# Kernel tuning notes

Measured on AMD Instinct MI355X. Metric: run time of the kernel, lower is better.

Reference implementation:

```python
import jax, jax.numpy as jnp
import numpy as np

N_NODES = 50000


def gcn_conv(x, W, b, src, dst, num_nodes):
    """PyG GCNConv: x' = D^{-1/2} (A + I) D^{-1/2} (x W) + b.

    Transform first (smaller feature dim work is the same either way here),
    then propagate with symmetric normalization including self-loops.
    """
    h = x @ W  # [N, F_out]
    # degree with self-loops: deg[i] = 1 + #incoming edges
    ones = jnp.ones(dst.shape[0], dtype=h.dtype)
    deg = jax.ops.segment_sum(ones, dst, num_segments=num_nodes) + 1.0  # [N]
    dinv_sqrt = jax.lax.rsqrt(deg)
    norm = dinv_sqrt[src] * dinv_sqrt[dst]  # [E]
    msg = h[src] * norm[:, None]  # [E, F_out]
    agg = jax.ops.segment_sum(msg, dst, num_segments=num_nodes)
    # self-loop contribution: norm_ii = deg_i^{-1/2} * deg_i^{-1/2} = 1/deg_i
    agg = agg + h * (dinv_sqrt * dinv_sqrt)[:, None]
    return agg + b


def setup_inputs() -> dict:
    key = jax.random.key(0)
    ks = jax.random.split(key, 11)
    N, E = N_NODES, 1600000
    in_ch, oc = 128, 32
    dims = [in_ch, 8 * oc, 4 * oc, 2 * oc, oc]  # 128 -> 256 -> 128 -> 64 -> 32
    x = jax.random.normal(ks[0], (N, in_ch), dtype=jnp.float32)
    edge_index = jax.random.randint(ks[1], (2, E), 0, N, dtype=jnp.int64)
    params = {}
    for i, (din, dout) in enumerate(zip(dims[:-1], dims[1:])):
        scale = 1.0 / np.sqrt(din)
        params[f"W{i+1}"] = jax.random.uniform(ks[2 + 2 * i], (din, dout), jnp.float32, -scale, scale)
        params[f"b{i+1}"] = jnp.zeros((dout,), dtype=jnp.float32)
    return {"x": x, "edge_index": edge_index, **params}


def reference(x, edge_index, W1, b1, W2, b2, W3, b3, W4, b4):
    src, dst = edge_index[0], edge_index[1]
    h = jax.nn.relu(gcn_conv(x, W1, b1, src, dst, N_NODES))
    h = jax.nn.relu(gcn_conv(h, W2, b2, src, dst, N_NODES))
    h = jax.nn.relu(gcn_conv(h, W3, b3, src, dst, N_NODES))
    h = jax.nn.relu(gcn_conv(h, W4, b4, src, dst, N_NODES))
    # Dropout(p=0.5) is identity at eval time.
    return h
```

## Files before the change

### kernel.cpp

```cpp
#include <hip/hip_runtime.h>
#include <stdint.h>


#define NN      50000
#define CAP     96
#define BSZ     256
#define NB      196
#define NSLICEA 256
#define CAPSEG  96
#define NBIN    16
#define LPAD    98

#define PREP_DINV_B   196
#define PREP_B2FS_B   6250
#define PREP_WT_T     2368
#define PREP_WT_B     10

typedef int   iv4   __attribute__((ext_vector_type(4)));
typedef short bfv8  __attribute__((ext_vector_type(8)));
typedef float fv4   __attribute__((ext_vector_type(4)));

__device__ __forceinline__ float bflo(uint32_t u) {
    uint32_t b = u << 16; float f; __builtin_memcpy(&f, &b, 4); return f;
}
__device__ __forceinline__ float bfhi(uint32_t u) {
    uint32_t b = u & 0xffff0000u; float f; __builtin_memcpy(&f, &b, 4); return f;
}
__device__ __forceinline__ unsigned short f2bf(float f) {
    uint32_t u; __builtin_memcpy(&u, &f, 4);
    return (unsigned short)((u + 0x7fffu + ((u >> 16) & 1u)) >> 16);
}
__device__ __forceinline__ uint32_t packbf(float lo, float hi) {
    return (uint32_t)f2bf(lo) | ((uint32_t)f2bf(hi) << 16);
}

__global__ __launch_bounds__(256) void k_bucket(uint32_t* __restrict__ seg,
                                                int* __restrict__ cnts,
                                                const int* __restrict__ src,
                                                const int* __restrict__ dst,
                                                int E) {
    __shared__ int cnt[NB];
    const int slice = blockIdx.x;
    for (int i = threadIdx.x; i < NB; i += 256) cnt[i] = 0;
    __syncthreads();
    int per = (E + NSLICEA - 1) / NSLICEA;
    per = (per + 3) & ~3;
    const int e0 = slice * per;
    uint32_t* const segp = seg + (long)slice * NB * CAPSEG;
    if (e0 < E) {
        const int e1 = (e0 + per < E) ? e0 + per : E;
        const int nv = (e1 - e0) & ~3;
        for (int t = e0 + (int)threadIdx.x * 4; t + 4 <= e0 + nv; t += 256 * 4) {
            iv4 dd = __builtin_nontemporal_load((const iv4*)(dst + t));
            iv4 ss = __builtin_nontemporal_load((const iv4*)(src + t));
#pragma unroll
            for (int q = 0; q < 4; ++q) {
                int d = dd[q];
                int b = d >> 8;
                uint32_t val = ((uint32_t)ss[q] << 8) | (uint32_t)(d & 255);
                int slot = atomicAdd(&cnt[b], 1);
                if (slot < CAPSEG) segp[b * CAPSEG + slot] = val;
            }
        }
        int tt = e0 + nv + (int)threadIdx.x;
        if (tt < e1) {
            int d = __builtin_nontemporal_load(dst + tt);
            int s = __builtin_nontemporal_load(src + tt);
            int b = d >> 8;
            uint32_t val = ((uint32_t)s << 8) | (uint32_t)(d & 255);
            int slot = atomicAdd(&cnt[b], 1);
            if (slot < CAPSEG) segp[b * CAPSEG + slot] = val;
        }
    }
    __syncthreads();
    for (int i = threadIdx.x; i < NB; i += 256)
        cnts[slice * NB + i] = (cnt[i] < CAPSEG) ? cnt[i] : CAPSEG;
}

__global__ __launch_bounds__(256) void k_build(unsigned short* __restrict__ pcsr,
                                               int* __restrict__ cur,
                                               const uint32_t* __restrict__ seg,
                                               const int* __restrict__ cnts,
                                               int N) {
    __shared__ unsigned short lrow[BSZ][LPAD];
    __shared__ int bcnt[BSZ][NBIN + 1];
    __shared__ int ldeg[BSZ];
    const int b = blockIdx.x;
    for (int i = threadIdx.x; i < BSZ * (NBIN + 1); i += 256)
        ((int*)bcnt)[i] = 0;
    __syncthreads();

    const int slice = threadIdx.x;
    const int n = cnts[slice * NB + b];
    const uint32_t* sp = seg + ((long)slice * NB + b) * CAPSEG;

    for (int i = 0; i < n; ++i) {
        uint32_t val = sp[i];
        int d = (int)(val & 255u);
        int s = (int)(val >> 8);
        atomicAdd(&bcnt[d][s >> 12], 1);
    }
    __syncthreads();

    {
        const int r = threadIdx.x;
        int acc = 0;
#pragma unroll
        for (int k = 0; k < NBIN; ++k) {
            int c = bcnt[r][k];
            bcnt[r][k] = acc;
            acc += c;
        }
        ldeg[r] = acc;
    }
    __syncthreads();

    for (int i = 0; i < n; ++i) {
        uint32_t val = sp[i];
        int d = (int)(val & 255u);
        int s = (int)(val >> 8);
        int slot = atomicAdd(&bcnt[d][s >> 12], 1);
        if (slot < CAP) lrow[d][slot] = (unsigned short)s;
    }
    __syncthreads();

    const int node0 = b * BSZ;
    int nrows = N - node0;
    if (nrows > BSZ) nrows = BSZ;
    const int total = nrows * (CAP / 2);
    for (int idx = threadIdx.x; idx < total; idx += 256) {
        int r = idx / (CAP / 2);
        int c = idx - r * (CAP / 2);
        ((uint32_t*)(pcsr + (long)(node0 + r) * CAP))[c] =
            ((const uint32_t*)lrow[r])[c];
    }
    for (int r = threadIdx.x; r < nrows; r += 256) cur[node0 + r] = ldeg[r];
}

__device__ __forceinline__ void wt_pack(unsigned short* __restrict__ wt,
                                        const float* __restrict__ W,
                                        int dout, int t) {
    int kc = t / dout, n = t - kc * dout;
    unsigned short* o = wt + (long)t * 32;
#pragma unroll
    for (int kk = 0; kk < 32; ++kk) o[kk] = f2bf(W[(kc * 32 + kk) * dout + n]);
}

__global__ __launch_bounds__(256) void k_prep(float* __restrict__ dinv,
                                              const int* __restrict__ cur,
                                              unsigned short* __restrict__ U,
                                              const float* __restrict__ x,
                                              unsigned short* __restrict__ Wt1,
                                              const float* __restrict__ W1,
                                              unsigned short* __restrict__ Wt2,
                                              const float* __restrict__ W2,
                                              unsigned short* __restrict__ Wt3,
                                              const float* __restrict__ W3,
                                              unsigned short* __restrict__ Wt4,
                                              const float* __restrict__ W4) {
    const int b = blockIdx.x;
    if (b < PREP_DINV_B) {
        int t = b * 256 + threadIdx.x;
        if (t < NN) dinv[t] = 1.0f / sqrtf((float)cur[t] + 1.0f);
    } else if (b < PREP_DINV_B + PREP_B2FS_B) {
        int t = (b - PREP_DINV_B) * 256 + threadIdx.x;
        float w = 1.0f / sqrtf((float)cur[t >> 5] + 1.0f);
        float4 v = reinterpret_cast<const float4*>(x)[t];
        ushort4 o;
        o.x = f2bf(v.x * w); o.y = f2bf(v.y * w);
        o.z = f2bf(v.z * w); o.w = f2bf(v.w * w);
        reinterpret_cast<ushort4*>(U)[t] = o;
    } else {
        int t = (b - PREP_DINV_B - PREP_B2FS_B) * 256 + threadIdx.x;
        if (t < 1024)      wt_pack(Wt1, W1, 256, t);
        else if (t < 2048) wt_pack(Wt2, W2, 128, t - 1024);
        else if (t < 2304) wt_pack(Wt3, W3, 64, t - 2048);
        else if (t < PREP_WT_T) wt_pack(Wt4, W4, 32, t - 2304);
    }
}

template <int D, int BR, int OUTBF>
__global__ __launch_bounds__(256) void k_pullq(void* __restrict__ outv,
                                               const unsigned short* __restrict__ Hb,
                                               const unsigned short* __restrict__ pcsr,
                                               const int* __restrict__ deg,
                                               const float* __restrict__ dinv,
                                               const float* __restrict__ bias,
                                               int n) {
    constexpr int TPN = D / 8;
    constexpr int NPB = 256 / TPN;
    const int node = blockIdx.x * NPB + threadIdx.x / TPN;
    const int f8 = threadIdx.x % TPN;
    if (node >= n) return;
    const float wd = dinv[node];
    const uint4* __restrict__ Hv = (const uint4*)Hb;
    uint4 ps = Hv[(long)node * TPN + f8];
    float a0 = bflo(ps.x), a1 = bfhi(ps.x);
    float a2 = bflo(ps.y), a3 = bfhi(ps.y);
    float a4 = bflo(ps.z), a5 = bfhi(ps.z);
    float a6 = bflo(ps.w), a7 = bfhi(ps.w);
    int dg = deg[node];
    if (dg > CAP) dg = CAP;
    const unsigned short* __restrict__ row = pcsr + (long)node * CAP;
    int j = 0;
    for (; j + 4 <= dg; j += 4) {
        ushort4 ii = *(const ushort4*)(row + j);
        uint4 p0 = Hv[(long)ii.x * TPN + f8];
        uint4 p1 = Hv[(long)ii.y * TPN + f8];
        uint4 p2 = Hv[(long)ii.z * TPN + f8];
        uint4 p3 = Hv[(long)ii.w * TPN + f8];
        a0 += bflo(p0.x) + bflo(p1.x) + bflo(p2.x) + bflo(p3.x);
        a1 += bfhi(p0.x) + bfhi(p1.x) + bfhi(p2.x) + bfhi(p3.x);
        a2 += bflo(p0.y) + bflo(p1.y) + bflo(p2.y) + bflo(p3.y);
        a3 += bfhi(p0.y) + bfhi(p1.y) + bfhi(p2.y) + bfhi(p3.y);
        a4 += bflo(p0.z) + bflo(p1.z) + bflo(p2.z) + bflo(p3.z);
        a5 += bfhi(p0.z) + bfhi(p1.z) + bfhi(p2.z) + bfhi(p3.z);
        a6 += bflo(p0.w) + bflo(p1.w) + bflo(p2.w) + bflo(p3.w);
        a7 += bfhi(p0.w) + bfhi(p1.w) + bfhi(p2.w) + bfhi(p3.w);
    }
    for (; j < dg; ++j) {
        uint4 p = Hv[(long)row[j] * TPN + f8];
        a0 += bflo(p.x); a1 += bfhi(p.x);
        a2 += bflo(p.y); a3 += bfhi(p.y);
        a4 += bflo(p.z); a5 += bfhi(p.z);
        a6 += bflo(p.w); a7 += bfhi(p.w);
    }
    a0 *= wd; a1 *= wd; a2 *= wd; a3 *= wd;
    a4 *= wd; a5 *= wd; a6 *= wd; a7 *= wd;
    if (BR) {
        float4 b0 = ((const float4*)bias)[2 * f8];
        float4 b1 = ((const float4*)bias)[2 * f8 + 1];
        a0 = fmaxf(a0 + b0.x, 0.f); a1 = fmaxf(a1 + b0.y, 0.f);
        a2 = fmaxf(a2 + b0.z, 0.f); a3 = fmaxf(a3 + b0.w, 0.f);
        a4 = fmaxf(a4 + b1.x, 0.f); a5 = fmaxf(a5 + b1.y, 0.f);
        a6 = fmaxf(a6 + b1.z, 0.f); a7 = fmaxf(a7 + b1.w, 0.f);
    }
    if (OUTBF) {
        uint4 o;
        o.x = packbf(a0, a1); o.y = packbf(a2, a3);
        o.z = packbf(a4, a5); o.w = packbf(a6, a7);
        ((uint4*)outv)[(long)node * TPN + f8] = o;
    } else {
        float4 o0; o0.x = a0; o0.y = a1; o0.z = a2; o0.w = a3;
        float4 o1; o1.x = a4; o1.y = a5; o1.z = a6; o1.w = a7;
        ((float4*)outv)[(long)node * (D / 4) + 2 * f8] = o0;
        ((float4*)outv)[(long)node * (D / 4) + 2 * f8 + 1] = o1;
    }
}

template <int DIN, int NT, int BIAS_RELU, int OUTBF, int SCALE>
__global__ __launch_bounds__(256) void k_mm(const unsigned short* __restrict__ Xb,
                                            const unsigned short* __restrict__ Wt,
                                            const float* __restrict__ bias,
                                            const float* __restrict__ dinv,
                                            void* __restrict__ outv,
                                            int N, int dout) {
    constexpr int KI = DIN / 32;
    const int lane = threadIdx.x & 63;
    const int wv   = threadIdx.x >> 6;
    const int m0   = blockIdx.x * 64 + wv * 16;
    const int n0   = blockIdx.y * (NT * 16);
    const int l15  = lane & 15;
    const int quad = lane >> 4;

    int mrow = m0 + l15;
    if (mrow >= N) mrow = N - 1;
    const unsigned short* xp = Xb + (long)mrow * DIN + quad * 8;
    const unsigned short* wp = Wt + (long)(n0 + l15) * 32 + quad * 8;

    fv4 acc[NT];
#pragma unroll
    for (int t = 0; t < NT; ++t) acc[t] = (fv4){0.f, 0.f, 0.f, 0.f};

#pragma unroll
    for (int kc = 0; kc < KI; ++kc) {
        bfv8 a = *(const bfv8*)(xp + kc * 32);
#pragma unroll
        for (int t = 0; t < NT; ++t) {
            bfv8 b = *(const bfv8*)(wp + (long)kc * dout * 32 + t * 16 * 32);
            acc[t] = __builtin_amdgcn_mfma_f32_16x16x32_bf16(a, b, acc[t], 0, 0, 0);
        }
    }

    float sc[4];
#pragma unroll
    for (int r = 0; r < 4; ++r) {
        int m = m0 + quad * 4 + r;
        sc[r] = SCALE ? dinv[(m < N) ? m : (N - 1)] : 1.0f;
    }

#pragma unroll
    for (int t = 0; t < NT; ++t) {
        const int col = n0 + t * 16 + l15;
        float bb = BIAS_RELU ? bias[col] : 0.f;
#pragma unroll
        for (int r = 0; r < 4; ++r) {
            int m = m0 + quad * 4 + r;
            if (m < N) {
                float v = acc[t][r];
                if (BIAS_RELU) v = fmaxf(v + bb, 0.f);
                if (SCALE) v *= sc[r];
                if (OUTBF)
                    ((unsigned short*)outv)[(long)m * dout + col] = f2bf(v);
                else
                    ((float*)outv)[(long)m * dout + col] = v;
            }
        }
    }
}

extern "C" void kernel_launch(void* const* d_in, const int* in_sizes, int n_in,
                              void* d_out, int out_size, void* d_ws, size_t ws_size,
                              hipStream_t stream) {
    const int N = NN;
    const int E = in_sizes[1] / 2;

    const float* x  = (const float*)d_in[0];
    const int* ei   = (const int*)d_in[1];
    const int* src  = ei;
    const int* dst  = ei + E;
    const float* W1 = (const float*)d_in[2];
    const float* b1 = (const float*)d_in[3];
    const float* W2 = (const float*)d_in[4];
    const float* b2 = (const float*)d_in[5];
    const float* W3 = (const float*)d_in[6];
    const float* b3 = (const float*)d_in[7];
    const float* W4 = (const float*)d_in[8];
    const float* b4 = (const float*)d_in[9];

    float* dinv = (float*)d_ws;
    int*   cur  = (int*)(dinv + N);
    unsigned short* U    = (unsigned short*)(cur + N);
    unsigned short* V    = U + (long)N * 256;
    unsigned short* pcsr = V + (long)N * 256;
    unsigned short* Wt1  = pcsr + (long)N * CAP;
    unsigned short* Wt2  = Wt1 + 128 * 256;
    unsigned short* Wt3  = Wt2 + 256 * 128;
    unsigned short* Wt4  = Wt3 + 128 * 64;

    uint32_t* seg  = (uint32_t*)U;
    int*      cnts = (int*)(seg + (long)NSLICEA * NB * CAPSEG);

    (void)n_in; (void)out_size; (void)ws_size;

    const int GX = (N + 63) / 64;

    k_bucket<<<NSLICEA, 256, 0, stream>>>(seg, cnts, src, dst, E);
    k_build<<<NB, 256, 0, stream>>>(pcsr, cur, seg, cnts, N);
    k_prep<<<PREP_DINV_B + PREP_B2FS_B + PREP_WT_B, 256, 0, stream>>>(
        dinv, cur, U, x, Wt1, W1, Wt2, W2, Wt3, W3, Wt4, W4);

    k_pullq<128, 0, 1><<<(N + 15) / 16, 256, 0, stream>>>(V, U, pcsr, cur, dinv, nullptr, N);
    k_mm<128, 4, 1, 1, 0><<<dim3(GX, 4), 256, 0, stream>>>(V, Wt1, b1, dinv, U, N, 256);

    k_mm<256, 4, 0, 1, 1><<<dim3(GX, 2), 256, 0, stream>>>(U, Wt2, nullptr, dinv, V, N, 128);
    k_pullq<128, 1, 1><<<(N + 15) / 16, 256, 0, stream>>>(U, V, pcsr, cur, dinv, b2, N);

    k_mm<128, 4, 0, 1, 1><<<dim3(GX, 1), 256, 0, stream>>>(U, Wt3, nullptr, dinv, V, N, 64);
    k_pullq<64, 1, 1><<<(N + 31) / 32, 256, 0, stream>>>(U, V, pcsr, cur, dinv, b3, N);

    k_mm<64, 2, 0, 1, 1><<<dim3(GX, 1), 256, 0, stream>>>(U, Wt4, nullptr, dinv, V, N, 32);
    k_pullq<32, 1, 0><<<(N + 63) / 64, 256, 0, stream>>>(d_out, V, pcsr, cur, dinv, b4, N);
}
```

Measured before the change: 308.6 us.

## Fuse layer-1 aggregation with its matmul and interleave two nodes per thread

Adds a kernel that gathers neighbour features for 32 nodes, stages the normalised bf16 rows in shared memory, and runs the 128->256 MFMA matmul with bias and ReLU in the same block. This removes the layer-1 intermediate write and read to global memory and one kernel launch. The 128-wide aggregation for layer 2 now gives each thread two nodes and interleaves their gathers to keep more loads in flight. The cost is fewer nodes per block in the fused kernel and heavier register and LDS use, which may lower occupancy, and the final output is written with scattered 2-byte stores.

```diff
diff --git a/kernel.cpp b/kernel.cpp
--- a/kernel.cpp
+++ b/kernel.cpp
@@ -10,6 +10,7 @@
 #define CAPSEG  96
 #define NBIN    16
 #define LPAD    98
+#define LSTR    68
 
 #define PREP_DINV_B   196
 #define PREP_B2FS_B   6250
@@ -96,12 +97,9 @@
 
     for (int i = 0; i < n; ++i) {
         uint32_t val = sp[i];
-        int d = (int)(val & 255u);
-        int s = (int)(val >> 8);
-        atomicAdd(&bcnt[d][s >> 12], 1);
-    }
-    __syncthreads();
-
+        atomicAdd(&bcnt[val & 255u][(val >> 8) >> 12], 1);
+    }
+    __syncthreads();
     {
         const int r = threadIdx.x;
         int acc = 0;
@@ -114,7 +112,6 @@
         ldeg[r] = acc;
     }
     __syncthreads();
-
     for (int i = 0; i < n; ++i) {
         uint32_t val = sp[i];
         int d = (int)(val & 255u);
@@ -179,6 +176,185 @@
     }
 }
 
+template <int TPN>
+__device__ __forceinline__ void gather4(const uint4* __restrict__ Hv,
+                                        const unsigned short* __restrict__ row,
+                                        int j, int f8, float* a) {
+    ushort4 ii = *(const ushort4*)(row + j);
+    uint4 p0 = Hv[(long)ii.x * TPN + f8];
+    uint4 p1 = Hv[(long)ii.y * TPN + f8];
+    uint4 p2 = Hv[(long)ii.z * TPN + f8];
+    uint4 p3 = Hv[(long)ii.w * TPN + f8];
+    a[0] += bflo(p0.x) + bflo(p1.x) + bflo(p2.x) + bflo(p3.x);
+    a[1] += bfhi(p0.x) + bfhi(p1.x) + bfhi(p2.x) + bfhi(p3.x);
+    a[2] += bflo(p0.y) + bflo(p1.y) + bflo(p2.y) + bflo(p3.y);
+    a[3] += bfhi(p0.y) + bfhi(p1.y) + bfhi(p2.y) + bfhi(p3.y);
+    a[4] += bflo(p0.z) + bflo(p1.z) + bflo(p2.z) + bflo(p3.z);
+    a[5] += bfhi(p0.z) + bfhi(p1.z) + bfhi(p2.z) + bfhi(p3.z);
+    a[6] += bflo(p0.w) + bflo(p1.w) + bflo(p2.w) + bflo(p3.w);
+    a[7] += bfhi(p0.w) + bfhi(p1.w) + bfhi(p2.w) + bfhi(p3.w);
+}
+template <int TPN>
+__device__ __forceinline__ void gather1(const uint4* __restrict__ Hv,
+                                        const unsigned short* __restrict__ row,
+                                        int j, int f8, float* a) {
+    uint4 p = Hv[(long)row[j] * TPN + f8];
+    a[0] += bflo(p.x); a[1] += bfhi(p.x);
+    a[2] += bflo(p.y); a[3] += bfhi(p.y);
+    a[4] += bflo(p.z); a[5] += bfhi(p.z);
+    a[6] += bflo(p.w); a[7] += bfhi(p.w);
+}
+
+__device__ __forceinline__ void pull2_core(const uint4* __restrict__ Hv,
+                                           const unsigned short* __restrict__ pcsr,
+                                           const int* __restrict__ deg,
+                                           int nA, int nB, int n, int f8,
+                                           float* aA, float* aB) {
+    int dgA = 0, dgB = 0;
+    const unsigned short *rowA = pcsr, *rowB = pcsr;
+    if (nA < n) {
+        uint4 ps = Hv[(long)nA * 16 + f8];
+        aA[0] = bflo(ps.x); aA[1] = bfhi(ps.x); aA[2] = bflo(ps.y); aA[3] = bfhi(ps.y);
+        aA[4] = bflo(ps.z); aA[5] = bfhi(ps.z); aA[6] = bflo(ps.w); aA[7] = bfhi(ps.w);
+        dgA = deg[nA]; if (dgA > CAP) dgA = CAP;
+        rowA = pcsr + (long)nA * CAP;
+    }
+    if (nB < n) {
+        uint4 ps = Hv[(long)nB * 16 + f8];
+        aB[0] = bflo(ps.x); aB[1] = bfhi(ps.x); aB[2] = bflo(ps.y); aB[3] = bfhi(ps.y);
+        aB[4] = bflo(ps.z); aB[5] = bfhi(ps.z); aB[6] = bflo(ps.w); aB[7] = bfhi(ps.w);
+        dgB = deg[nB]; if (dgB > CAP) dgB = CAP;
+        rowB = pcsr + (long)nB * CAP;
+    }
+    int ja = 0, jb = 0;
+    while (ja + 4 <= dgA && jb + 4 <= dgB) {
+        gather4<16>(Hv, rowA, ja, f8, aA); ja += 4;
+        gather4<16>(Hv, rowB, jb, f8, aB); jb += 4;
+    }
+    for (; ja + 4 <= dgA; ja += 4) gather4<16>(Hv, rowA, ja, f8, aA);
+    for (; jb + 4 <= dgB; jb += 4) gather4<16>(Hv, rowB, jb, f8, aB);
+    for (; ja < dgA; ++ja) gather1<16>(Hv, rowA, ja, f8, aA);
+    for (; jb < dgB; ++jb) gather1<16>(Hv, rowB, jb, f8, aB);
+}
+
+template <int BR, int OUTBF>
+__global__ __launch_bounds__(256) void k_pullq2(void* __restrict__ outv,
+                                                const unsigned short* __restrict__ Hb,
+                                                const unsigned short* __restrict__ pcsr,
+                                                const int* __restrict__ deg,
+                                                const float* __restrict__ dinv,
+                                                const float* __restrict__ bias,
+                                                int n) {
+    const int slot = threadIdx.x >> 4;
+    const int f8   = threadIdx.x & 15;
+    const int base = blockIdx.x * 32;
+    const int nA = base + slot, nB = base + slot + 16;
+    const uint4* __restrict__ Hv = (const uint4*)Hb;
+    float aA[8] = {0,0,0,0,0,0,0,0}, aB[8] = {0,0,0,0,0,0,0,0};
+    pull2_core(Hv, pcsr, deg, nA, nB, n, f8, aA, aB);
+
+    float b8[8];
+    if (BR) {
+        float4 b0 = ((const float4*)bias)[2 * f8];
+        float4 b1 = ((const float4*)bias)[2 * f8 + 1];
+        b8[0] = b0.x; b8[1] = b0.y; b8[2] = b0.z; b8[3] = b0.w;
+        b8[4] = b1.x; b8[5] = b1.y; b8[6] = b1.z; b8[7] = b1.w;
+    }
+#pragma unroll
+    for (int pass = 0; pass < 2; ++pass) {
+        int node = pass ? nB : nA;
+        float* a = pass ? aB : aA;
+        if (node >= n) continue;
+        float wd = dinv[node];
+#pragma unroll
+        for (int k = 0; k < 8; ++k) {
+            a[k] *= wd;
+            if (BR) a[k] = fmaxf(a[k] + b8[k], 0.f);
+        }
+        if (OUTBF) {
+            uint4 o;
+            o.x = packbf(a[0], a[1]); o.y = packbf(a[2], a[3]);
+            o.z = packbf(a[4], a[5]); o.w = packbf(a[6], a[7]);
+            ((uint4*)outv)[(long)node * 16 + f8] = o;
+        } else {
+            float4 o0 = {a[0], a[1], a[2], a[3]};
+            float4 o1 = {a[4], a[5], a[6], a[7]};
+            ((float4*)outv)[(long)node * 32 + 2 * f8] = o0;
+            ((float4*)outv)[(long)node * 32 + 2 * f8 + 1] = o1;
+        }
+    }
+}
+
+__global__ __launch_bounds__(256) void k_pullmm1(unsigned short* __restrict__ outH,
+                                                 const unsigned short* __restrict__ Hb,
+                                                 const unsigned short* __restrict__ pcsr,
+                                                 const int* __restrict__ deg,
+                                                 const float* __restrict__ dinv,
+                                                 const unsigned short* __restrict__ Wt,
+                                                 const float* __restrict__ bias,
+                                                 int n) {
+    __shared__ uint32_t lds[32 * LSTR];
+    const int slot = threadIdx.x >> 4;
+    const int f8   = threadIdx.x & 15;
+    const int base = blockIdx.x * 32;
+    const int nA = base + slot, nB = base + slot + 16;
+    const uint4* __restrict__ Hv = (const uint4*)Hb;
+    float aA[8] = {0,0,0,0,0,0,0,0}, aB[8] = {0,0,0,0,0,0,0,0};
+    pull2_core(Hv, pcsr, deg, nA, nB, n, f8, aA, aB);
+
+    {
+        float wdA = (nA < n) ? dinv[nA] : 0.f;
+        float wdB = (nB < n) ? dinv[nB] : 0.f;
+        uint32_t* pa = &lds[slot * LSTR + f8 * 4];
+        uint32_t* pb = &lds[(slot + 16) * LSTR + f8 * 4];
+        pa[0] = packbf(aA[0] * wdA, aA[1] * wdA);
+        pa[1] = packbf(aA[2] * wdA, aA[3] * wdA);
+        pa[2] = packbf(aA[4] * wdA, aA[5] * wdA);
+        pa[3] = packbf(aA[6] * wdA, aA[7] * wdA);
+        pb[0] = packbf(aB[0] * wdB, aB[1] * wdB);
+        pb[1] = packbf(aB[2] * wdB, aB[3] * wdB);
+        pb[2] = packbf(aB[4] * wdB, aB[5] * wdB);
+        pb[3] = packbf(aB[6] * wdB, aB[7] * wdB);
+    }
+    __syncthreads();
+
+    const int lane = threadIdx.x & 63;
+    const int wv   = threadIdx.x >> 6;
+    const int l15  = lane & 15;
+    const int quad = lane >> 4;
+    const int n0   = wv * 64;
+    fv4 acc[2][4];
+#pragma unroll
+    for (int mt = 0; mt < 2; ++mt)
+#pragma unroll
+        for (int t = 0; t < 4; ++t) acc[mt][t] = (fv4){0.f, 0.f, 0.f, 0.f};
+
+#pragma unroll
+    for (int kc = 0; kc < 4; ++kc) {
+        bfv8 a0 = *(const bfv8*)((const unsigned short*)&lds[l15 * LSTR] + quad * 8 + kc * 32);
+        bfv8 a1 = *(const bfv8*)((const unsigned short*)&lds[(16 + l15) * LSTR] + quad * 8 + kc * 32);
+#pragma unroll
+        for (int t = 0; t < 4; ++t) {
+            bfv8 b = *(const bfv8*)(Wt + (long)(n0 + t * 16 + l15) * 32 + quad * 8 + (long)kc * 256 * 32);
+            acc[0][t] = __builtin_amdgcn_mfma_f32_16x16x32_bf16(a0, b, acc[0][t], 0, 0, 0);
+            acc[1][t] = __builtin_amdgcn_mfma_f32_16x16x32_bf16(a1, b, acc[1][t], 0, 0, 0);
+        }
+    }
+#pragma unroll
+    for (int mt = 0; mt < 2; ++mt)
+#pragma unroll
+        for (int t = 0; t < 4; ++t) {
+            int col = n0 + t * 16 + l15;
+            float bb = bias[col];
+#pragma unroll
+            for (int r = 0; r < 4; ++r) {
+                int m = base + mt * 16 + quad * 4 + r;
+                if (m < n)
+                    outH[(long)m * 256 + col] = f2bf(fmaxf(acc[mt][t][r] + bb, 0.f));
+            }
+        }
+}
+
 template <int D, int BR, int OUTBF>
 __global__ __launch_bounds__(256) void k_pullq(void* __restrict__ outv,
                                                const unsigned short* __restrict__ Hb,
@@ -195,54 +371,33 @@
     const float wd = dinv[node];
     const uint4* __restrict__ Hv = (const uint4*)Hb;
     uint4 ps = Hv[(long)node * TPN + f8];
-    float a0 = bflo(ps.x), a1 = bfhi(ps.x);
-    float a2 = bflo(ps.y), a3 = bfhi(ps.y);
-    float a4 = bflo(ps.z), a5 = bfhi(ps.z);
-    float a6 = bflo(ps.w), a7 = bfhi(ps.w);
+    float a[8];
+    a[0] = bflo(ps.x); a[1] = bfhi(ps.x); a[2] = bflo(ps.y); a[3] = bfhi(ps.y);
+    a[4] = bflo(ps.z); a[5] = bfhi(ps.z); a[6] = bflo(ps.w); a[7] = bfhi(ps.w);
     int dg = deg[node];
     if (dg > CAP) dg = CAP;
     const unsigned short* __restrict__ row = pcsr + (long)node * CAP;
     int j = 0;
-    for (; j + 4 <= dg; j += 4) {
-        ushort4 ii = *(const ushort4*)(row + j);
-        uint4 p0 = Hv[(long)ii.x * TPN + f8];
-        uint4 p1 = Hv[(long)ii.y * TPN + f8];
-        uint4 p2 = Hv[(long)ii.z * TPN + f8];
-        uint4 p3 = Hv[(long)ii.w * TPN + f8];
-        a0 += bflo(p0.x) + bflo(p1.x) + bflo(p2.x) + bflo(p3.x);
-        a1 += bfhi(p0.x) + bfhi(p1.x) + bfhi(p2.x) + bfhi(p3.x);
-        a2 += bflo(p0.y) + bflo(p1.y) + bflo(p2.y) + bflo(p3.y);
-        a3 += bfhi(p0.y) + bfhi(p1.y) + bfhi(p2.y) + bfhi(p3.y);
-        a4 += bflo(p0.z) + bflo(p1.z) + bflo(p2.z) + bflo(p3.z);
-        a5 += bfhi(p0.z) + bfhi(p1.z) + bfhi(p2.z) + bfhi(p3.z);
-        a6 += bflo(p0.w) + bflo(p1.w) + bflo(p2.w) + bflo(p3.w);
-        a7 += bfhi(p0.w) + bfhi(p1.w) + bfhi(p2.w) + bfhi(p3.w);
-    }
-    for (; j < dg; ++j) {
-        uint4 p = Hv[(long)row[j] * TPN + f8];
-        a0 += bflo(p.x); a1 += bfhi(p.x);
-        a2 += bflo(p.y); a3 += bfhi(p.y);
-        a4 += bflo(p.z); a5 += bfhi(p.z);
-        a6 += bflo(p.w); a7 += bfhi(p.w);
-    }
-    a0 *= wd; a1 *= wd; a2 *= wd; a3 *= wd;
-    a4 *= wd; a5 *= wd; a6 *= wd; a7 *= wd;
+    for (; j + 4 <= dg; j += 4) gather4<TPN>(Hv, row, j, f8, a);
+    for (; j < dg; ++j) gather1<TPN>(Hv, row, j, f8, a);
+#pragma unroll
+    for (int k = 0; k < 8; ++k) a[k] *= wd;
     if (BR) {
         float4 b0 = ((const float4*)bias)[2 * f8];
         float4 b1 = ((const float4*)bias)[2 * f8 + 1];
-        a0 = fmaxf(a0 + b0.x, 0.f); a1 = fmaxf(a1 + b0.y, 0.f);
-        a2 = fmaxf(a2 + b0.z, 0.f); a3 = fmaxf(a3 + b0.w, 0.f);
-        a4 = fmaxf(a4 + b1.x, 0.f); a5 = fmaxf(a5 + b1.y, 0.f);
-        a6 = fmaxf(a6 + b1.z, 0.f); a7 = fmaxf(a7 + b1.w, 0.f);
+        a[0] = fmaxf(a[0] + b0.x, 0.f); a[1] = fmaxf(a[1] + b0.y, 0.f);
+        a[2] = fmaxf(a[2] + b0.z, 0.f); a[3] = fmaxf(a[3] + b0.w, 0.f);
+        a[4] = fmaxf(a[4] + b1.x, 0.f); a[5] = fmaxf(a[5] + b1.y, 0.f);
+        a[6] = fmaxf(a[6] + b1.z, 0.f); a[7] = fmaxf(a[7] + b1.w, 0.f);
     }
     if (OUTBF) {
         uint4 o;
-        o.x = packbf(a0, a1); o.y = packbf(a2, a3);
-        o.z = packbf(a4, a5); o.w = packbf(a6, a7);
+        o.x = packbf(a[0], a[1]); o.y = packbf(a[2], a[3]);
+        o.z = packbf(a[4], a[5]); o.w = packbf(a[6], a[7]);
         ((uint4*)outv)[(long)node * TPN + f8] = o;
     } else {
-        float4 o0; o0.x = a0; o0.y = a1; o0.z = a2; o0.w = a3;
-        float4 o1; o1.x = a4; o1.y = a5; o1.z = a6; o1.w = a7;
+        float4 o0 = {a[0], a[1], a[2], a[3]};
+        float4 o1 = {a[4], a[5], a[6], a[7]};
         ((float4*)outv)[(long)node * (D / 4) + 2 * f8] = o0;
         ((float4*)outv)[(long)node * (D / 4) + 2 * f8 + 1] = o1;
     }
@@ -344,21 +499,21 @@
     (void)n_in; (void)out_size; (void)ws_size;
 
     const int GX = (N + 63) / 64;
+    const int GP2 = (N + 31) / 32;
 
     k_bucket<<<NSLICEA, 256, 0, stream>>>(seg, cnts, src, dst, E);
     k_build<<<NB, 256, 0, stream>>>(pcsr, cur, seg, cnts, N);
     k_prep<<<PREP_DINV_B + PREP_B2FS_B + PREP_WT_B, 256, 0, stream>>>(
         dinv, cur, U, x, Wt1, W1, Wt2, W2, Wt3, W3, Wt4, W4);
 
-    k_pullq<128, 0, 1><<<(N + 15) / 16, 256, 0, stream>>>(V, U, pcsr, cur, dinv, nullptr, N);
-    k_mm<128, 4, 1, 1, 0><<<dim3(GX, 4), 256, 0, stream>>>(V, Wt1, b1, dinv, U, N, 256);
-
-    k_mm<256, 4, 0, 1, 1><<<dim3(GX, 2), 256, 0, stream>>>(U, Wt2, nullptr, dinv, V, N, 128);
-    k_pullq<128, 1, 1><<<(N + 15) / 16, 256, 0, stream>>>(U, V, pcsr, cur, dinv, b2, N);
-
-    k_mm<128, 4, 0, 1, 1><<<dim3(GX, 1), 256, 0, stream>>>(U, Wt3, nullptr, dinv, V, N, 64);
-    k_pullq<64, 1, 1><<<(N + 31) / 32, 256, 0, stream>>>(U, V, pcsr, cur, dinv, b3, N);
-
-    k_mm<64, 2, 0, 1, 1><<<dim3(GX, 1), 256, 0, stream>>>(U, Wt4, nullptr, dinv, V, N, 32);
-    k_pullq<32, 1, 0><<<(N + 63) / 64, 256, 0, stream>>>(d_out, V, pcsr, cur, dinv, b4, N);
-}
+    k_pullmm1<<<GP2, 256, 0, stream>>>(V, U, pcsr, cur, dinv, Wt1, b1, N);
+
+    k_mm<256, 4, 0, 1, 1><<<dim3(GX, 2), 256, 0, stream>>>(V, Wt2, nullptr, dinv, U, N, 128);
+    k_pullq2<1, 1><<<GP2, 256, 0, stream>>>(V, U, pcsr, cur, dinv, b2, N);
+
+    k_mm<128, 4, 0, 1, 1><<<dim3(GX, 1), 256, 0, stream>>>(V, Wt3, nullptr, dinv, U, N, 64);
+    k_pullq<64, 1, 1><<<(N + 31) / 32, 256, 0, stream>>>(V, U, pcsr, cur, dinv, b3, N);
+
+    k_mm<64, 2, 0, 1, 1><<<dim3(GX, 1), 256, 0, stream>>>(V, Wt4, nullptr, dinv, U, N, 32);
+    k_pullq<32, 1, 0><<<(N + 63) / 64, 256, 0, stream>>>(d_out, U, pcsr, cur, dinv, b4, N);
+}
```

Result: slower. 324.9 us (+5.3%).

## Fuse prep, propagation and matmul stages into one cooperative persistent kernel

Applied to the files above, without the earlier changes.

Replaces the nine separate prep/pull/matmul launches with a single cooperative kernel that loops over virtual blocks and uses grid-wide syncs between stages. The aim is to remove per-launch overhead and the tail idle time at each kernel boundary. The grid size comes from an occupancy query with a minimum-occupancy hint of five blocks per CU, and the old multi-launch path is kept as a fallback if the cooperative launch fails. In exchange, grid.sync costs are added, __restrict__ qualifiers are dropped, and the fused kernel may suffer higher register pressure.

```diff
diff --git a/kernel.cpp b/kernel.cpp
--- a/kernel.cpp
+++ b/kernel.cpp
@@ -1,5 +1,8 @@
 #include <hip/hip_runtime.h>
+#include <hip/hip_cooperative_groups.h>
 #include <stdint.h>
+
+namespace cg = cooperative_groups;
 
 
 #define NN      50000
@@ -15,6 +18,12 @@
 #define PREP_B2FS_B   6250
 #define PREP_WT_T     2368
 #define PREP_WT_B     10
+#define PREP_TOT_B    (PREP_DINV_B + PREP_B2FS_B + PREP_WT_B)
+
+#define GXMM    782
+#define VB_P128 3125
+#define VB_P64  1563
+#define VB_P32  782
 
 typedef int   iv4   __attribute__((ext_vector_type(4)));
 typedef short bfv8  __attribute__((ext_vector_type(8)));
@@ -96,12 +105,9 @@
 
     for (int i = 0; i < n; ++i) {
         uint32_t val = sp[i];
-        int d = (int)(val & 255u);
-        int s = (int)(val >> 8);
-        atomicAdd(&bcnt[d][s >> 12], 1);
-    }
-    __syncthreads();
-
+        atomicAdd(&bcnt[val & 255u][(val >> 8) >> 12], 1);
+    }
+    __syncthreads();
     {
         const int r = threadIdx.x;
         int acc = 0;
@@ -114,7 +120,6 @@
         ldeg[r] = acc;
     }
     __syncthreads();
-
     for (int i = 0; i < n; ++i) {
         uint32_t val = sp[i];
         int d = (int)(val & 255u);
@@ -137,8 +142,7 @@
     for (int r = threadIdx.x; r < nrows; r += 256) cur[node0 + r] = ldeg[r];
 }
 
-__device__ __forceinline__ void wt_pack(unsigned short* __restrict__ wt,
-                                        const float* __restrict__ W,
+__device__ __forceinline__ void wt_pack(unsigned short* wt, const float* W,
                                         int dout, int t) {
     int kc = t / dout, n = t - kc * dout;
     unsigned short* o = wt + (long)t * 32;
@@ -146,24 +150,18 @@
     for (int kk = 0; kk < 32; ++kk) o[kk] = f2bf(W[(kc * 32 + kk) * dout + n]);
 }
 
-__global__ __launch_bounds__(256) void k_prep(float* __restrict__ dinv,
-                                              const int* __restrict__ cur,
-                                              unsigned short* __restrict__ U,
-                                              const float* __restrict__ x,
-                                              unsigned short* __restrict__ Wt1,
-                                              const float* __restrict__ W1,
-                                              unsigned short* __restrict__ Wt2,
-                                              const float* __restrict__ W2,
-                                              unsigned short* __restrict__ Wt3,
-                                              const float* __restrict__ W3,
-                                              unsigned short* __restrict__ Wt4,
-                                              const float* __restrict__ W4) {
-    const int b = blockIdx.x;
+__device__ __forceinline__ void prep_body(int b, int tid,
+                                          float* dinv, const int* cur,
+                                          unsigned short* U, const float* x,
+                                          unsigned short* Wt1, const float* W1,
+                                          unsigned short* Wt2, const float* W2,
+                                          unsigned short* Wt3, const float* W3,
+                                          unsigned short* Wt4, const float* W4) {
     if (b < PREP_DINV_B) {
-        int t = b * 256 + threadIdx.x;
+        int t = b * 256 + tid;
         if (t < NN) dinv[t] = 1.0f / sqrtf((float)cur[t] + 1.0f);
     } else if (b < PREP_DINV_B + PREP_B2FS_B) {
-        int t = (b - PREP_DINV_B) * 256 + threadIdx.x;
+        int t = (b - PREP_DINV_B) * 256 + tid;
         float w = 1.0f / sqrtf((float)cur[t >> 5] + 1.0f);
         float4 v = reinterpret_cast<const float4*>(x)[t];
         ushort4 o;
@@ -171,7 +169,7 @@
         o.z = f2bf(v.z * w); o.w = f2bf(v.w * w);
         reinterpret_cast<ushort4*>(U)[t] = o;
     } else {
-        int t = (b - PREP_DINV_B - PREP_B2FS_B) * 256 + threadIdx.x;
+        int t = (b - PREP_DINV_B - PREP_B2FS_B) * 256 + tid;
         if (t < 1024)      wt_pack(Wt1, W1, 256, t);
         else if (t < 2048) wt_pack(Wt2, W2, 128, t - 1024);
         else if (t < 2304) wt_pack(Wt3, W3, 64, t - 2048);
@@ -179,87 +177,95 @@
     }
 }
 
+template <int TPN>
+__device__ __forceinline__ void gather4(const uint4* Hv,
+                                        const unsigned short* row,
+                                        int j, int f8, float* a) {
+    ushort4 ii = *(const ushort4*)(row + j);
+    uint4 p0 = Hv[(long)ii.x * TPN + f8];
+    uint4 p1 = Hv[(long)ii.y * TPN + f8];
+    uint4 p2 = Hv[(long)ii.z * TPN + f8];
+    uint4 p3 = Hv[(long)ii.w * TPN + f8];
+    a[0] += bflo(p0.x) + bflo(p1.x) + bflo(p2.x) + bflo(p3.x);
+    a[1] += bfhi(p0.x) + bfhi(p1.x) + bfhi(p2.x) + bfhi(p3.x);
+    a[2] += bflo(p0.y) + bflo(p1.y) + bflo(p2.y) + bflo(p3.y);
+    a[3] += bfhi(p0.y) + bfhi(p1.y) + bfhi(p2.y) + bfhi(p3.y);
+    a[4] += bflo(p0.z) + bflo(p1.z) + bflo(p2.z) + bflo(p3.z);
+    a[5] += bfhi(p0.z) + bfhi(p1.z) + bfhi(p2.z) + bfhi(p3.z);
+    a[6] += bflo(p0.w) + bflo(p1.w) + bflo(p2.w) + bflo(p3.w);
+    a[7] += bfhi(p0.w) + bfhi(p1.w) + bfhi(p2.w) + bfhi(p3.w);
+}
+template <int TPN>
+__device__ __forceinline__ void gather1(const uint4* Hv,
+                                        const unsigned short* row,
+                                        int j, int f8, float* a) {
+    uint4 p = Hv[(long)row[j] * TPN + f8];
+    a[0] += bflo(p.x); a[1] += bfhi(p.x);
+    a[2] += bflo(p.y); a[3] += bfhi(p.y);
+    a[4] += bflo(p.z); a[5] += bfhi(p.z);
+    a[6] += bflo(p.w); a[7] += bfhi(p.w);
+}
+
 template <int D, int BR, int OUTBF>
-__global__ __launch_bounds__(256) void k_pullq(void* __restrict__ outv,
-                                               const unsigned short* __restrict__ Hb,
-                                               const unsigned short* __restrict__ pcsr,
-                                               const int* __restrict__ deg,
-                                               const float* __restrict__ dinv,
-                                               const float* __restrict__ bias,
-                                               int n) {
+__device__ __forceinline__ void pull_body(int vb, int tid,
+                                          void* outv,
+                                          const unsigned short* Hb,
+                                          const unsigned short* pcsr,
+                                          const int* deg,
+                                          const float* dinv,
+                                          const float* bias, int n) {
     constexpr int TPN = D / 8;
     constexpr int NPB = 256 / TPN;
-    const int node = blockIdx.x * NPB + threadIdx.x / TPN;
-    const int f8 = threadIdx.x % TPN;
+    const int node = vb * NPB + tid / TPN;
+    const int f8 = tid % TPN;
     if (node >= n) return;
     const float wd = dinv[node];
-    const uint4* __restrict__ Hv = (const uint4*)Hb;
+    const uint4* Hv = (const uint4*)Hb;
     uint4 ps = Hv[(long)node * TPN + f8];
-    float a0 = bflo(ps.x), a1 = bfhi(ps.x);
-    float a2 = bflo(ps.y), a3 = bfhi(ps.y);
-    float a4 = bflo(ps.z), a5 = bfhi(ps.z);
-    float a6 = bflo(ps.w), a7 = bfhi(ps.w);
+    float a[8];
+    a[0] = bflo(ps.x); a[1] = bfhi(ps.x); a[2] = bflo(ps.y); a[3] = bfhi(ps.y);
+    a[4] = bflo(ps.z); a[5] = bfhi(ps.z); a[6] = bflo(ps.w); a[7] = bfhi(ps.w);
     int dg = deg[node];
     if (dg > CAP) dg = CAP;
-    const unsigned short* __restrict__ row = pcsr + (long)node * CAP;
+    const unsigned short* row = pcsr + (long)node * CAP;
     int j = 0;
-    for (; j + 4 <= dg; j += 4) {
-        ushort4 ii = *(const ushort4*)(row + j);
-        uint4 p0 = Hv[(long)ii.x * TPN + f8];
-        uint4 p1 = Hv[(long)ii.y * TPN + f8];
-        uint4 p2 = Hv[(long)ii.z * TPN + f8];
-        uint4 p3 = Hv[(long)ii.w * TPN + f8];
-        a0 += bflo(p0.x) + bflo(p1.x) + bflo(p2.x) + bflo(p3.x);
-        a1 += bfhi(p0.x) + bfhi(p1.x) + bfhi(p2.x) + bfhi(p3.x);
-        a2 += bflo(p0.y) + bflo(p1.y) + bflo(p2.y) + bflo(p3.y);
-        a3 += bfhi(p0.y) + bfhi(p1.y) + bfhi(p2.y) + bfhi(p3.y);
-        a4 += bflo(p0.z) + bflo(p1.z) + bflo(p2.z) + bflo(p3.z);
-        a5 += bfhi(p0.z) + bfhi(p1.z) + bfhi(p2.z) + bfhi(p3.z);
-        a6 += bflo(p0.w) + bflo(p1.w) + bflo(p2.w) + bflo(p3.w);
-        a7 += bfhi(p0.w) + bfhi(p1.w) + bfhi(p2.w) + bfhi(p3.w);
-    }
-    for (; j < dg; ++j) {
-        uint4 p = Hv[(long)row[j] * TPN + f8];
-        a0 += bflo(p.x); a1 += bfhi(p.x);
-        a2 += bflo(p.y); a3 += bfhi(p.y);
-        a4 += bflo(p.z); a5 += bfhi(p.z);
-        a6 += bflo(p.w); a7 += bfhi(p.w);
-    }
-    a0 *= wd; a1 *= wd; a2 *= wd; a3 *= wd;
-    a4 *= wd; a5 *= wd; a6 *= wd; a7 *= wd;
+    for (; j + 4 <= dg; j += 4) gather4<TPN>(Hv, row, j, f8, a);
+    for (; j < dg; ++j) gather1<TPN>(Hv, row, j, f8, a);
+#pragma unroll
+    for (int k = 0; k < 8; ++k) a[k] *= wd;
     if (BR) {
         float4 b0 = ((const float4*)bias)[2 * f8];
         float4 b1 = ((const float4*)bias)[2 * f8 + 1];
-        a0 = fmaxf(a0 + b0.x, 0.f); a1 = fmaxf(a1 + b0.y, 0.f);
-        a2 = fmaxf(a2 + b0.z, 0.f); a3 = fmaxf(a3 + b0.w, 0.f);
-        a4 = fmaxf(a4 + b1.x, 0.f); a5 = fmaxf(a5 + b1.y, 0.f);
-        a6 = fmaxf(a6 + b1.z, 0.f); a7 = fmaxf(a7 + b1.w, 0.f);
+        a[0] = fmaxf(a[0] + b0.x, 0.f); a[1] = fmaxf(a[1] + b0.y, 0.f);
+        a[2] = fmaxf(a[2] + b0.z, 0.f); a[3] = fmaxf(a[3] + b0.w, 0.f);
+        a[4] = fmaxf(a[4] + b1.x, 0.f); a[5] = fmaxf(a[5] + b1.y, 0.f);
+        a[6] = fmaxf(a[6] + b1.z, 0.f); a[7] = fmaxf(a[7] + b1.w, 0.f);
     }
     if (OUTBF) {
         uint4 o;
-        o.x = packbf(a0, a1); o.y = packbf(a2, a3);
-        o.z = packbf(a4, a5); o.w = packbf(a6, a7);
+        o.x = packbf(a[0], a[1]); o.y = packbf(a[2], a[3]);
+        o.z = packbf(a[4], a[5]); o.w = packbf(a[6], a[7]);
         ((uint4*)outv)[(long)node * TPN + f8] = o;
     } else {
-        float4 o0; o0.x = a0; o0.y = a1; o0.z = a2; o0.w = a3;
-        float4 o1; o1.x = a4; o1.y = a5; o1.z = a6; o1.w = a7;
+        float4 o0 = {a[0], a[1], a[2], a[3]};
+        float4 o1 = {a[4], a[5], a[6], a[7]};
         ((float4*)outv)[(long)node * (D / 4) + 2 * f8] = o0;
         ((float4*)outv)[(long)node * (D / 4) + 2 * f8 + 1] = o1;
     }
 }
 
 template <int DIN, int NT, int BIAS_RELU, int OUTBF, int SCALE>
-__global__ __launch_bounds__(256) void k_mm(const unsigned short* __restrict__ Xb,
-                                            const unsigned short* __restrict__ Wt,
-                                            const float* __restrict__ bias,
-                                            const float* __restrict__ dinv,
-                                            void* __restrict__ outv,
-                                            int N, int dout) {
+__device__ __forceinline__ void mm_body(int bx, int by, int tid,
+                                        const unsigned short* Xb,
+                                        const unsigned short* Wt,
+                                        const float* bias,
+                                        const float* dinv,
+                                        void* outv, int N, int dout) {
     constexpr int KI = DIN / 32;
-    const int lane = threadIdx.x & 63;
-    const int wv   = threadIdx.x >> 6;
-    const int m0   = blockIdx.x * 64 + wv * 16;
-    const int n0   = blockIdx.y * (NT * 16);
+    const int lane = tid & 63;
+    const int wv   = tid >> 6;
+    const int m0   = bx * 64 + wv * 16;
+    const int n0   = by * (NT * 16);
     const int l15  = lane & 15;
     const int quad = lane >> 4;
 
@@ -309,6 +315,70 @@
     }
 }
 
+__global__ __launch_bounds__(256, 5) void k_mega(
+        float* dinv, const int* cur, unsigned short* U, unsigned short* V,
+        const unsigned short* pcsr, const float* x,
+        unsigned short* Wt1, unsigned short* Wt2,
+        unsigned short* Wt3, unsigned short* Wt4,
+        const float* W1, const float* W2, const float* W3, const float* W4,
+        const float* b1, const float* b2, const float* b3, const float* b4,
+        float* outF, int N) {
+    cg::grid_group grid = cg::this_grid();
+    const int tid = threadIdx.x;
+    const int nblk = gridDim.x;
+
+    for (int b = blockIdx.x; b < PREP_TOT_B; b += nblk)
+        prep_body(b, tid, dinv, cur, U, x, Wt1, W1, Wt2, W2, Wt3, W3, Wt4, W4);
+    grid.sync();
+    for (int vb = blockIdx.x; vb < VB_P128; vb += nblk)
+        pull_body<128, 0, 1>(vb, tid, V, U, pcsr, cur, dinv, nullptr, N);
+    grid.sync();
+    for (int vb = blockIdx.x; vb < GXMM * 4; vb += nblk)
+        mm_body<128, 4, 1, 1, 0>(vb % GXMM, vb / GXMM, tid, V, Wt1, b1, dinv, U, N, 256);
+    grid.sync();
+    for (int vb = blockIdx.x; vb < GXMM * 2; vb += nblk)
+        mm_body<256, 4, 0, 1, 1>(vb % GXMM, vb / GXMM, tid, U, Wt2, nullptr, dinv, V, N, 128);
+    grid.sync();
+    for (int vb = blockIdx.x; vb < VB_P128; vb += nblk)
+        pull_body<128, 1, 1>(vb, tid, U, V, pcsr, cur, dinv, b2, N);
+    grid.sync();
+    for (int vb = blockIdx.x; vb < GXMM; vb += nblk)
+        mm_body<128, 4, 0, 1, 1>(vb, 0, tid, U, Wt3, nullptr, dinv, V, N, 64);
+    grid.sync();
+    for (int vb = blockIdx.x; vb < VB_P64; vb += nblk)
+        pull_body<64, 1, 1>(vb, tid, U, V, pcsr, cur, dinv, b3, N);
+    grid.sync();
+    for (int vb = blockIdx.x; vb < GXMM; vb += nblk)
+        mm_body<64, 2, 0, 1, 1>(vb, 0, tid, U, Wt4, nullptr, dinv, V, N, 32);
+    grid.sync();
+    for (int vb = blockIdx.x; vb < VB_P32; vb += nblk)
+        pull_body<32, 1, 0>(vb, tid, outF, V, pcsr, cur, dinv, b4, N);
+}
+
+__global__ __launch_bounds__(256) void k_prep(float* dinv, const int* cur,
+                                              unsigned short* U, const float* x,
+                                              unsigned short* Wt1, const float* W1,
+                                              unsigned short* Wt2, const float* W2,
+                                              unsigned short* Wt3, const float* W3,
+                                              unsigned short* Wt4, const float* W4) {
+    prep_body(blockIdx.x, threadIdx.x, dinv, cur, U, x, Wt1, W1, Wt2, W2, Wt3, W3, Wt4, W4);
+}
+template <int D, int BR, int OUTBF>
+__global__ __launch_bounds__(256) void k_pullq(void* outv, const unsigned short* Hb,
+                                               const unsigned short* pcsr,
+                                               const int* deg, const float* dinv,
+                                               const float* bias, int n) {
+    pull_body<D, BR, OUTBF>(blockIdx.x, threadIdx.x, outv, Hb, pcsr, deg, dinv, bias, n);
+}
+template <int DIN, int NT, int BIAS_RELU, int OUTBF, int SCALE>
+__global__ __launch_bounds__(256) void k_mm(const unsigned short* Xb,
+                                            const unsigned short* Wt,
+                                            const float* bias, const float* dinv,
+                                            void* outv, int N, int dout) {
+    mm_body<DIN, NT, BIAS_RELU, OUTBF, SCALE>(blockIdx.x, blockIdx.y, threadIdx.x,
+                                              Xb, Wt, bias, dinv, outv, N, dout);
+}
+
 extern "C" void kernel_launch(void* const* d_in, const int* in_sizes, int n_in,
                               void* d_out, int out_size, void* d_ws, size_t ws_size,
                               hipStream_t stream) {
@@ -343,22 +413,41 @@
 
     (void)n_in; (void)out_size; (void)ws_size;
 
-    const int GX = (N + 63) / 64;
-
     k_bucket<<<NSLICEA, 256, 0, stream>>>(seg, cnts, src, dst, E);
     k_build<<<NB, 256, 0, stream>>>(pcsr, cur, seg, cnts, N);
-    k_prep<<<PREP_DINV_B + PREP_B2FS_B + PREP_WT_B, 256, 0, stream>>>(
-        dinv, cur, U, x, Wt1, W1, Wt2, W2, Wt3, W3, Wt4, W4);
-
-    k_pullq<128, 0, 1><<<(N + 15) / 16, 256, 0, stream>>>(V, U, pcsr, cur, dinv, nullptr, N);
-    k_mm<128, 4, 1, 1, 0><<<dim3(GX, 4), 256, 0, stream>>>(V, Wt1, b1, dinv, U, N, 256);
-
-    k_mm<256, 4, 0, 1, 1><<<dim3(GX, 2), 256, 0, stream>>>(U, Wt2, nullptr, dinv, V, N, 128);
-    k_pullq<128, 1, 1><<<(N + 15) / 16, 256, 0, stream>>>(U, V, pcsr, cur, dinv, b2, N);
-
-    k_mm<128, 4, 0, 1, 1><<<dim3(GX, 1), 256, 0, stream>>>(U, Wt3, nullptr, dinv, V, N, 64);
-    k_pullq<64, 1, 1><<<(N + 31) / 32, 256, 0, stream>>>(U, V, pcsr, cur, dinv, b3, N);
-
-    k_mm<64, 2, 0, 1, 1><<<dim3(GX, 1), 256, 0, stream>>>(U, Wt4, nullptr, dinv, V, N, 32);
-    k_pullq<32, 1, 0><<<(N + 63) / 64, 256, 0, stream>>>(d_out, V, pcsr, cur, dinv, b4, N);
-}
+
+    static int G = 0;
+    if (G == 0) {
+        int nb = 0;
+        if (hipOccupancyMaxActiveBlocksPerMultiprocessor(&nb, k_mega, 256, 0)
+                != hipSuccess || nb < 1)
+            nb = 4;
+        G = nb * 256;
+        if (G > VB_P128) G = VB_P128;
+    }
+    float* outF = (float*)d_out;
+    unsigned short *uU = U, *uV = V;
+    const unsigned short* cpcsr = pcsr;
+    int nN = N;
+    void* args[] = {
+        &dinv, &cur, &uU, &uV, &cpcsr, &x,
+        &Wt1, &Wt2, &Wt3, &Wt4,
+        &W1, &W2, &W3, &W4,
+        &b1, &b2, &b3, &b4,
+        &outF, &nN };
+    hipError_t err = hipLaunchCooperativeKernel((const void*)k_mega,
+                                                dim3(G), dim3(256), args, 0, stream);
+    if (err != hipSuccess) {
+        const int GX = GXMM;
+        k_prep<<<PREP_TOT_B, 256, 0, stream>>>(dinv, cur, U, x, Wt1, W1, Wt2, W2,
+                                               Wt3, W3, Wt4, W4);
+        k_pullq<128, 0, 1><<<VB_P128, 256, 0, stream>>>(V, U, pcsr, cur, dinv, nullptr, N);
+        k_mm<128, 4, 1, 1, 0><<<dim3(GX, 4), 256, 0, stream>>>(V, Wt1, b1, dinv, U, N, 256);
+        k_mm<256, 4, 0, 1, 1><<<dim3(GX, 2), 256, 0, stream>>>(U, Wt2, nullptr, dinv, V, N, 128);
+        k_pullq<128, 1, 1><<<VB_P128, 256, 0, stream>>>(U, V, pcsr, cur, dinv, b2, N);
+        k_mm<128, 4, 0, 1, 1><<<dim3(GX, 1), 256, 0, stream>>>(U, Wt3, nullptr, dinv, V, N, 64);
+        k_pullq<64, 1, 1><<<VB_P64, 256, 0, stream>>>(U, V, pcsr, cur, dinv, b3, N);
+        k_mm<64, 2, 0, 1, 1><<<dim3(GX, 1), 256, 0, stream>>>(U, Wt4, nullptr, dinv, V, N, 32);
+        k_pullq<32, 1, 0><<<VB_P32, 256, 0, stream>>>(d_out, V, pcsr, cur, dinv, b4, N);
+    }
+}
```

After: 1.120 ms. 263% more time.
